# Kernel tuning notes

Measured on AMD Instinct MI355X. Metric: run time of the kernel, lower is better.

## Reference

```python
import jax, jax.numpy as jnp
import numpy as np

B, T, F_DIM, HID, CH = 16, 4096, 47, 64, 256  # batch, frames, feature_dim, hidden_feature_dim, num_channels


def setup_inputs() -> dict:
    key = jax.random.key(0)
    ks = jax.random.split(key, 8)
    s = 0.08  # weight scale
    return {
        "features": jax.random.normal(ks[0], (B, T, F_DIM), jnp.float32),
        # conv1: Conv1d(47, 64, k=1) -> pointwise linear, torch weight (out,in,1) squeezed
        "W1": jax.random.normal(ks[1], (HID, F_DIM), jnp.float32) * s,
        "b1": jnp.zeros((HID,), jnp.float32),
        # conv2: Conv1d(256, 256, k=2), torch weight (out, in, k)
        "W2": jax.random.normal(ks[2], (CH, 4 * HID, 2), jnp.float32) * s,
        "b2": jnp.zeros((CH,), jnp.float32),
        # tconv: ConvTranspose1d(256, 256, k=4, stride=4), torch weight (in, out, k)
        "Wt": jax.random.normal(ks[3], (CH, CH, 4), jnp.float32) * s,
        "bt": jnp.zeros((CH,), jnp.float32),
        # GRU(256, 256), torch layout: (3*H, in) with gate order [r, z, n]
        "W_ih": jax.random.normal(ks[4], (3 * CH, CH), jnp.float32) * s,
        "W_hh": jax.random.normal(ks[5], (3 * CH, CH), jnp.float32) * s,
        "b_ih": jnp.zeros((3 * CH,), jnp.float32),
        "b_hh": jnp.zeros((3 * CH,), jnp.float32),
    }


def reference(features, W1, b1, W2, b2, Wt, bt, W_ih, W_hh, b_ih, b_hh):
    b, t = features.shape[0], features.shape[1]
    ch = Wt.shape[1]
    # conv1 (k=1) == pointwise linear + tanh: (B,T,47) -> (B,T,64)
    c = jnp.tanh(jnp.einsum('btf,hf->bth', features, W1) + b1)
    # group 4 frames: (B, T/4, 256)
    c = c.reshape(b, t // 4, -1)
    # conv2 k=2 with left pad 1 (causal): y[t] = W2[..0] x[t-1] + W2[..1] x[t]
    cp = jnp.pad(c, ((0, 0), (1, 0), (0, 0)))
    c = jnp.tanh(jnp.einsum('bti,oi->bto', cp[:, :-1], W2[:, :, 0])
                 + jnp.einsum('bti,oi->bto', cp[:, 1:], W2[:, :, 1]) + b2)
    # tconv: stride-4 transpose conv, k=4 -> each frame emits 4 steps
    c = jnp.tanh(jnp.einsum('bti,iok->btko', c, Wt) + bt)  # (B, T/4, 4, CH)
    c = c.reshape(b, t, ch)
    # GRU (torch semantics, gate order r,z,n); precompute input projections
    gates_x = jnp.einsum('btc,gc->btg', c, W_ih) + b_ih  # (B,T,3CH)

    def step(h, gx):
        gh = h @ W_hh.T + b_hh
        xr, xz, xn = jnp.split(gx, 3, axis=-1)
        hr, hz, hn = jnp.split(gh, 3, axis=-1)
        r = jax.nn.sigmoid(xr + hr)
        z = jax.nn.sigmoid(xz + hz)
        n = jnp.tanh(xn + r * hn)
        h = (1 - z) * n + z * h
        return h, h

    h0 = jnp.zeros((b, ch), features.dtype)
    _, hs = jax.lax.scan(step, h0, jnp.swapaxes(gates_x, 0, 1))  # (T,B,CH)
    return jnp.swapaxes(hs, 0, 1)  # (B,T,CH)
```

## Files before the change

### kernel.cpp

```cpp
#include <hip/hip_runtime.h>
#include <hip/hip_bf16.h>
#include <stdint.h>

#define B_   16
#define T_   4096
#define F_   47
#define HID_ 64
#define CH_  256
#define TG_  1024
#define G3_  768

using bf16x8 = __attribute__((ext_vector_type(8))) short;
using f32x4  = __attribute__((ext_vector_type(4))) float;

__device__ __forceinline__ short f2bf(float f) {
    union { float f; uint32_t u; } v; v.f = f;
    uint32_t u = v.u;
    uint32_t r = (u + 0x7fffu + ((u >> 16) & 1u)) >> 16;
    return (short)r;
}
__device__ __forceinline__ float bf2f(short s) {
    union { uint32_t u; float f; } v; v.u = ((uint32_t)(uint16_t)s) << 16;
    return v.f;
}
__device__ __forceinline__ float fast_tanh(float x) {
    float e = __expf(2.f * x);
    return 1.f - 2.f / (e + 1.f);
}
__device__ __forceinline__ float fast_sigmoid(float x) {
    return 1.f / (1.f + __expf(-x));
}

__global__ __launch_bounds__(256) void k1_conv1(const float* __restrict__ feat,
        const float* __restrict__ W1, const float* __restrict__ b1,
        short* __restrict__ c1) {
    __shared__ float sW[47 * 64];
    __shared__ float sF[4 * 47];
    int tid = threadIdx.x;
    int b = blockIdx.x >> 10, t0 = (blockIdx.x & 1023) * 4;
    if (tid < 188) sF[tid] = feat[((size_t)b * T_ + t0) * 47 + tid];
    for (int i = tid; i < 47 * 64; i += 256) {
        int f = i >> 6, h = i & 63;
        sW[i] = W1[h * 47 + f];
    }
    __syncthreads();
    int fr = tid >> 6, h = tid & 63;
    float acc = b1[h];
    #pragma unroll
    for (int f = 0; f < 47; ++f)
        acc += sF[fr * 47 + f] * sW[f * 64 + h];
    c1[((size_t)b * T_ + t0 + fr) * 64 + h] = f2bf(fast_tanh(acc));
}

__global__ __launch_bounds__(256) void k_prep(const float* __restrict__ W2,
        const float* __restrict__ Wt, const float* __restrict__ Wih_f,
        short* __restrict__ W2t, short* __restrict__ Wtt, short* __restrict__ Wih) {
    int idx = blockIdx.x * 256 + threadIdx.x;
    if (idx < 256 * 512) {
        int o = idx >> 9, i = idx & 511, d = i >> 8, j = i & 255;
        W2t[idx] = f2bf(W2[(size_t)o * 512 + j * 2 + d]);
    }
    {
        int n = idx >> 8, ic = idx & 255, o = n & 255, kp = n >> 8;
        Wtt[idx] = f2bf(Wt[(size_t)ic * 1024 + o * 4 + kp]);
    }
    if (idx < G3_ * CH_)
        Wih[idx] = f2bf(Wih_f[idx]);
}

__global__ __launch_bounds__(256) void k2_conv2(const short* __restrict__ c1,
        const short* __restrict__ W2t, const float* __restrict__ b2,
        short* __restrict__ y2) {
    int tid = threadIdx.x, w = tid >> 6, l = tid & 63;
    int lane16 = l & 15, quad = l >> 4;
    int mt = blockIdx.x * 4 + w;
    int row = mt * 16 + lane16;
    int tg = row & 1023;
    const short* Arow = c1 + (size_t)row * 256 - 256;
    bf16x8 zero8 = {0,0,0,0,0,0,0,0};
    bf16x8 af[16];
    #pragma unroll
    for (int kt = 0; kt < 16; ++kt) {
        int i0 = kt * 32 + quad * 8;
        bool masked = (tg == 0) && (kt < 8);
        const short* p = masked ? c1 : (Arow + i0);
        bf16x8 v = *(const bf16x8*)p;
        af[kt] = masked ? zero8 : v;
    }
    #pragma unroll
    for (int nt = 0; nt < 16; ++nt) {
        int n = nt * 16 + lane16;
        f32x4 acc = {0.f, 0.f, 0.f, 0.f};
        const short* Brow = W2t + (size_t)n * 512 + quad * 8;
        #pragma unroll
        for (int kt = 0; kt < 16; ++kt) {
            bf16x8 bf = *(const bf16x8*)(Brow + kt * 32);
            acc = __builtin_amdgcn_mfma_f32_16x16x32_bf16(af[kt], bf, acc, 0, 0, 0);
        }
        float bias = b2[n];
        #pragma unroll
        for (int r = 0; r < 4; ++r) {
            int mrow = mt * 16 + quad * 4 + r;
            y2[(size_t)mrow * 256 + n] = f2bf(fast_tanh(acc[r] + bias));
        }
    }
}

__global__ __launch_bounds__(256) void k3a_tconv(const short* __restrict__ y2,
        const short* __restrict__ Wtt, const float* __restrict__ bt,
        short* __restrict__ c3) {
    int tid = threadIdx.x, w = tid >> 6, l = tid & 63;
    int lane16 = l & 15, quad = l >> 4;
    int mt = blockIdx.x;
    int row = mt * 16 + lane16;
    const short* Arow = y2 + (size_t)row * 256 + quad * 8;
    bf16x8 af[8];
    #pragma unroll
    for (int kt = 0; kt < 8; ++kt) af[kt] = *(const bf16x8*)(Arow + kt * 32);
    #pragma unroll
    for (int nt2 = 0; nt2 < 16; ++nt2) {
        int n = (w * 16 + nt2) * 16 + lane16;
        f32x4 acc = {0.f, 0.f, 0.f, 0.f};
        const short* Brow = Wtt + (size_t)n * 256 + quad * 8;
        #pragma unroll
        for (int kt = 0; kt < 8; ++kt) {
            bf16x8 bf = *(const bf16x8*)(Brow + kt * 32);
            acc = __builtin_amdgcn_mfma_f32_16x16x32_bf16(af[kt], bf, acc, 0, 0, 0);
        }
        int kp = n >> 8, o = n & 255;
        float bias = bt[o];
        #pragma unroll
        for (int r = 0; r < 4; ++r) {
            int mrow = mt * 16 + quad * 4 + r;
            int bb = mrow >> 10, tgg = mrow & 1023;
            c3[(((size_t)bb * TG_ + tgg) * 4 + kp) * 256 + o] =
                f2bf(fast_tanh(acc[r] + bias));
        }
    }
}

__global__ __launch_bounds__(256) void k3b_xproj(const short* __restrict__ c3,
        const short* __restrict__ Wih, const float* __restrict__ b_ih,
        short* __restrict__ gates) {
    int tid = threadIdx.x, w = tid >> 6, l = tid & 63;
    int lane16 = l & 15, quad = l >> 4;
    int mt = blockIdx.x;
    int row = mt * 16 + lane16;
    const short* Arow = c3 + (size_t)row * 256 + quad * 8;
    bf16x8 af[8];
    #pragma unroll
    for (int kt = 0; kt < 8; ++kt) af[kt] = *(const bf16x8*)(Arow + kt * 32);
    #pragma unroll
    for (int nt2 = 0; nt2 < 12; ++nt2) {
        int n = (w * 12 + nt2) * 16 + lane16;
        f32x4 acc = {0.f, 0.f, 0.f, 0.f};
        const short* Brow = Wih + (size_t)n * 256 + quad * 8;
        #pragma unroll
        for (int kt = 0; kt < 8; ++kt) {
            bf16x8 bf = *(const bf16x8*)(Brow + kt * 32);
            acc = __builtin_amdgcn_mfma_f32_16x16x32_bf16(af[kt], bf, acc, 0, 0, 0);
        }
        float bias = b_ih[n];
        #pragma unroll
        for (int r = 0; r < 4; ++r) {
            int mrow = mt * 16 + quad * 4 + r;
            gates[(size_t)mrow * G3_ + n] = f2bf(acc[r] + bias);
        }
    }
}

__global__ __launch_bounds__(512, 2) void k4_gru(const float* __restrict__ W_hh,
        const float* __restrict__ b_hh, const short* __restrict__ gates,
        float* __restrict__ out) {
    __shared__ __align__(16) short h_bf[256];
    __shared__ float gh[G3_];
    __shared__ __align__(16) short gxb[2][8][G3_];
    __shared__ __align__(16) float ob[8][256];
    int tid = threadIdx.x, l = tid & 63;
    int w = tid >> 6;
    int lane16 = l & 15, quad = l >> 4;
    int b = blockIdx.x;

    bf16x8 Bfr[6][8];
    #pragma unroll
    for (int t = 0; t < 6; ++t) {
        int n = (w * 6 + t) * 16 + lane16;
        const float* p = W_hh + (size_t)n * 256 + quad * 8;
        #pragma unroll
        for (int kt = 0; kt < 8; ++kt) {
            const f32x4* q = (const f32x4*)(p + kt * 32);
            f32x4 u0 = q[0], u1 = q[1];
            bf16x8 v;
            v[0] = f2bf(u0[0]); v[1] = f2bf(u0[1]); v[2] = f2bf(u0[2]); v[3] = f2bf(u0[3]);
            v[4] = f2bf(u1[0]); v[5] = f2bf(u1[1]); v[6] = f2bf(u1[2]); v[7] = f2bf(u1[3]);
            Bfr[t][kt] = v;
        }
    }

    float h_reg = 0.f, bhr = 0.f, bhz = 0.f, bhn = 0.f;
    if (tid < 256) {
        h_bf[tid] = 0;
        bhr = b_hh[tid]; bhz = b_hh[256 + tid]; bhn = b_hh[512 + tid];
    }
    const uint32_t* gxg = (const uint32_t*)(gates + (size_t)b * T_ * G3_);
    if (tid < 384) {
        #pragma unroll
        for (int j = 0; j < 8; ++j)
            ((uint32_t*)&gxb[0][j][0])[tid] = gxg[(size_t)j * 384 + tid];
    }
    __syncthreads();

    float* outb = out + (size_t)b * T_ * CH_;
    uint32_t r[8];
    for (int s = 0; s < T_; ++s) {
        bool ldq = ((s & 7) == 0) && (s + 8 < T_) && (tid < 384);
        if (ldq) {
            #pragma unroll
            for (int j = 0; j < 8; ++j)
                r[j] = gxg[(size_t)(s + 8 + j) * 384 + tid];
        }

        f32x4 acc[6];
        #pragma unroll
        for (int t = 0; t < 6; ++t) acc[t] = (f32x4){0.f, 0.f, 0.f, 0.f};
        bf16x8 af[4];
        #pragma unroll
        for (int p = 0; p < 4; ++p)
            af[p] = *(const bf16x8*)&h_bf[p * 32 + quad * 8];
        #pragma unroll
        for (int kt = 0; kt < 8; ++kt) {
            bf16x8 a = af[kt & 3];
            if (kt + 4 < 8)
                af[kt & 3] = *(const bf16x8*)&h_bf[(kt + 4) * 32 + quad * 8];
            #pragma unroll
            for (int t = 0; t < 6; ++t)
                acc[t] = __builtin_amdgcn_mfma_f32_16x16x32_bf16(a, Bfr[t][kt], acc[t], 0, 0, 0);
        }
        if (l < 16) {
            #pragma unroll
            for (int t = 0; t < 6; ++t) gh[(w * 6 + t) * 16 + l] = acc[t][0];
        }
        __syncthreads();

        if (ldq) {
            int half = ((s >> 3) + 1) & 1;
            #pragma unroll
            for (int j = 0; j < 8; ++j)
                ((uint32_t*)&gxb[half][j][0])[tid] = r[j];
        }

        if (tid < 256) {
            const short* gx = &gxb[(s >> 3) & 1][s & 7][0];
            float hr = gh[tid] + bhr;
            float hz = gh[256 + tid] + bhz;
            float hn = gh[512 + tid] + bhn;
            float xr = bf2f(gx[tid]), xz = bf2f(gx[256 + tid]), xn = bf2f(gx[512 + tid]);
            float rg = fast_sigmoid(xr + hr);
            float z = fast_sigmoid(xz + hz);
            float nn = fast_tanh(xn + rg * hn);
            h_reg = (1.f - z) * nn + z * h_reg;
            h_bf[tid] = f2bf(h_reg);
            ob[s & 7][tid] = h_reg;
        }
        __syncthreads();

        if ((s & 7) == 7) {
            f32x4 v = *(const f32x4*)&ob[0][tid * 4];
            *(f32x4*)&outb[(size_t)(s - 7) * 256 + tid * 4] = v;
        }
    }
}

extern "C" void kernel_launch(void* const* d_in, const int* in_sizes, int n_in,
                              void* d_out, int out_size, void* d_ws, size_t ws_size,
                              hipStream_t stream) {
    const float* feat  = (const float*)d_in[0];
    const float* W1    = (const float*)d_in[1];
    const float* b1    = (const float*)d_in[2];
    const float* W2    = (const float*)d_in[3];
    const float* b2    = (const float*)d_in[4];
    const float* Wt    = (const float*)d_in[5];
    const float* bt    = (const float*)d_in[6];
    const float* Wih_f = (const float*)d_in[7];
    const float* Whh   = (const float*)d_in[8];
    const float* bhh   = (const float*)d_in[10];
    const float* bih   = (const float*)d_in[9];
    float* out = (float*)d_out;

    char* ws = (char*)d_ws;
    short* c3    = (short*)(ws);
    short* c1    = (short*)(ws);
    short* gates = (short*)(ws + 33554432);
    short* y2    = (short*)(ws + 33554432);
    short* W2t   = (short*)(ws + 134217728);
    short* Wtt   = (short*)(ws + 134217728 + 262144);
    short* Wih   = (short*)(ws + 134217728 + 262144 + 524288);

    k1_conv1 <<<16384, 256, 0, stream>>>(feat, W1, b1, c1);
    k_prep   <<<1024, 256, 0, stream>>>(W2, Wt, Wih_f, W2t, Wtt, Wih);
    k2_conv2 <<<256,  256, 0, stream>>>(c1, W2t, b2, y2);
    k3a_tconv<<<1024, 256, 0, stream>>>(y2, Wtt, bt, c3);
    k3b_xproj<<<4096, 256, 0, stream>>>(c3, Wih, bih, gates);
    k4_gru   <<<16,   512, 0, stream>>>(Whh, bhh, gates, out);
}
```

Baseline: 5.678 ms.

## Replace MFMA GRU recurrence with fp16 dot2 per-thread matvec and LDS-direct prefetch

```diff
diff --git a/kernel.cpp b/kernel.cpp
--- a/kernel.cpp
+++ b/kernel.cpp
@@ -12,6 +12,8 @@
 
 using bf16x8 = __attribute__((ext_vector_type(8))) short;
 using f32x4  = __attribute__((ext_vector_type(4))) float;
+using f16x8  = __attribute__((ext_vector_type(8))) _Float16;
+using h2     = __attribute__((ext_vector_type(2))) _Float16;
 
 __device__ __forceinline__ short f2bf(float f) {
     union { float f; uint32_t u; } v; v.f = f;
@@ -30,6 +32,26 @@
 __device__ __forceinline__ float fast_sigmoid(float x) {
     return 1.f / (1.f + __expf(-x));
 }
+
+#if __has_builtin(__builtin_amdgcn_fdot2)
+#define FDOT2(a, b, c) __builtin_amdgcn_fdot2((a), (b), (c), false)
+#else
+__device__ __forceinline__ float fdot2_emul(h2 a, h2 b, float c) {
+    return c + (float)a[0] * (float)b[0] + (float)a[1] * (float)b[1];
+}
+#define FDOT2(a, b, c) fdot2_emul((a), (b), (c))
+#endif
+
+#if __has_builtin(__builtin_amdgcn_global_load_lds)
+#define HAS_GLL 1
+__device__ __forceinline__ void gl_lds16(const void* g, void* l) {
+    __builtin_amdgcn_global_load_lds(
+        (const __attribute__((address_space(1))) uint32_t*)g,
+        (__attribute__((address_space(3))) uint32_t*)l, 16, 0, 0);
+}
+#else
+#define HAS_GLL 0
+#endif
 
 __global__ __launch_bounds__(256) void k1_conv1(const float* __restrict__ feat,
         const float* __restrict__ W1, const float* __restrict__ b1,
@@ -57,8 +79,8 @@
         short* __restrict__ W2t, short* __restrict__ Wtt, short* __restrict__ Wih) {
     int idx = blockIdx.x * 256 + threadIdx.x;
     if (idx < 256 * 512) {
-        int o = idx >> 9, i = idx & 511, d = i >> 8, j = i & 255;
-        W2t[idx] = f2bf(W2[(size_t)o * 512 + j * 2 + d]);
+        int o = idx >> 9, i = idx & 511, d = i >> 8, jj = i & 255;
+        W2t[idx] = f2bf(W2[(size_t)o * 512 + jj * 2 + d]);
     }
     {
         int n = idx >> 8, ic = idx & 255, o = n & 255, kp = n >> 8;
@@ -169,104 +191,125 @@
     }
 }
 
-__global__ __launch_bounds__(512, 2) void k4_gru(const float* __restrict__ W_hh,
+__global__ __launch_bounds__(512) void k4_gru_dot2(const float* __restrict__ W_hh,
         const float* __restrict__ b_hh, const short* __restrict__ gates,
         float* __restrict__ out) {
-    __shared__ __align__(16) short h_bf[256];
-    __shared__ float gh[G3_];
     __shared__ __align__(16) short gxb[2][8][G3_];
-    __shared__ __align__(16) float ob[8][256];
-    int tid = threadIdx.x, l = tid & 63;
-    int w = tid >> 6;
-    int lane16 = l & 15, quad = l >> 4;
+    __shared__ __align__(16) float part[G3_ * 4];
+    __shared__ __align__(16) float ob[8 * 256];
+    __shared__ __align__(16) short hq_s[4 * 72];
+
+    int tid = threadIdx.x, l = tid & 63, w = tid >> 6;
+    int q = tid & 3, n0 = tid >> 2;
     int b = blockIdx.x;
 
-    bf16x8 Bfr[6][8];
-    #pragma unroll
-    for (int t = 0; t < 6; ++t) {
-        int n = (w * 6 + t) * 16 + lane16;
-        const float* p = W_hh + (size_t)n * 256 + quad * 8;
-        #pragma unroll
-        for (int kt = 0; kt < 8; ++kt) {
-            const f32x4* q = (const f32x4*)(p + kt * 32);
-            f32x4 u0 = q[0], u1 = q[1];
-            bf16x8 v;
-            v[0] = f2bf(u0[0]); v[1] = f2bf(u0[1]); v[2] = f2bf(u0[2]); v[3] = f2bf(u0[3]);
-            v[4] = f2bf(u1[0]); v[5] = f2bf(u1[1]); v[6] = f2bf(u1[2]); v[7] = f2bf(u1[3]);
-            Bfr[t][kt] = v;
+    h2 wreg[6][32];
+    #pragma unroll
+    for (int k = 0; k < 6; ++k) {
+        const float2* row = (const float2*)(W_hh + ((size_t)(n0 + k * 128)) * 256 + q * 64);
+        #pragma unroll
+        for (int j = 0; j < 32; ++j) {
+            float2 v = row[j];
+            h2 p; p[0] = (_Float16)v.x; p[1] = (_Float16)v.y;
+            wreg[k][j] = p;
         }
     }
 
     float h_reg = 0.f, bhr = 0.f, bhz = 0.f, bhn = 0.f;
     if (tid < 256) {
-        h_bf[tid] = 0;
         bhr = b_hh[tid]; bhz = b_hh[256 + tid]; bhn = b_hh[512 + tid];
     }
-    const uint32_t* gxg = (const uint32_t*)(gates + (size_t)b * T_ * G3_);
-    if (tid < 384) {
-        #pragma unroll
-        for (int j = 0; j < 8; ++j)
-            ((uint32_t*)&gxb[0][j][0])[tid] = gxg[(size_t)j * 384 + tid];
-    }
+    if (tid < 288) hq_s[tid] = 0;
+
+    const short* gbase = gates + (size_t)b * T_ * G3_;
+    const char* gbytes = (const char*)gbase;
+
+#if HAS_GLL
+    {
+        char* dst = (char*)&gxb[0][0][0];
+        gl_lds16(gbytes + w * 1024 + l * 16, dst + w * 1024);
+        if (w < 4) gl_lds16(gbytes + (8 + w) * 1024 + l * 16, dst + (8 + w) * 1024);
+    }
+#else
+    {
+        const uint32_t* g32 = (const uint32_t*)gbytes;
+        uint32_t* d = (uint32_t*)&gxb[0][0][0];
+        #pragma unroll
+        for (int i = 0; i < 6; ++i) d[tid + i * 512] = g32[tid + i * 512];
+    }
+#endif
     __syncthreads();
 
     float* outb = out + (size_t)b * T_ * CH_;
-    uint32_t r[8];
     for (int s = 0; s < T_; ++s) {
-        bool ldq = ((s & 7) == 0) && (s + 8 < T_) && (tid < 384);
-        if (ldq) {
+        bool grp0 = ((s & 7) == 0) && (s + 8 < T_);
+#if HAS_GLL
+        if (grp0) {
+            const char* src = gbytes + (size_t)(s + 8) * 1536;
+            char* dst = (char*)&gxb[((s >> 3) + 1) & 1][0][0];
+            gl_lds16(src + w * 1024 + l * 16, dst + w * 1024);
+            if (w < 4) gl_lds16(src + (8 + w) * 1024 + l * 16, dst + (8 + w) * 1024);
+        }
+#else
+        uint32_t pf[6];
+        if (grp0) {
+            const uint32_t* src = (const uint32_t*)(gbytes + (size_t)(s + 8) * 1536);
             #pragma unroll
-            for (int j = 0; j < 8; ++j)
-                r[j] = gxg[(size_t)(s + 8 + j) * 384 + tid];
-        }
-
-        f32x4 acc[6];
-        #pragma unroll
-        for (int t = 0; t < 6; ++t) acc[t] = (f32x4){0.f, 0.f, 0.f, 0.f};
-        bf16x8 af[4];
-        #pragma unroll
-        for (int p = 0; p < 4; ++p)
-            af[p] = *(const bf16x8*)&h_bf[p * 32 + quad * 8];
-        #pragma unroll
-        for (int kt = 0; kt < 8; ++kt) {
-            bf16x8 a = af[kt & 3];
-            if (kt + 4 < 8)
-                af[kt & 3] = *(const bf16x8*)&h_bf[(kt + 4) * 32 + quad * 8];
+            for (int i = 0; i < 6; ++i) pf[i] = src[tid + i * 512];
+        }
+#endif
+
+        h2 hq[32];
+        #pragma unroll
+        for (int g2 = 0; g2 < 8; ++g2) {
+            f16x8 v = *(const f16x8*)&hq_s[q * 72 + g2 * 8];
             #pragma unroll
-            for (int t = 0; t < 6; ++t)
-                acc[t] = __builtin_amdgcn_mfma_f32_16x16x32_bf16(a, Bfr[t][kt], acc[t], 0, 0, 0);
-        }
-        if (l < 16) {
+            for (int p2 = 0; p2 < 4; ++p2) {
+                h2 p; p[0] = v[p2 * 2]; p[1] = v[p2 * 2 + 1];
+                hq[g2 * 4 + p2] = p;
+            }
+        }
+        float acc[6] = {0.f, 0.f, 0.f, 0.f, 0.f, 0.f};
+        #pragma unroll
+        for (int j = 0; j < 32; ++j) {
             #pragma unroll
-            for (int t = 0; t < 6; ++t) gh[(w * 6 + t) * 16 + l] = acc[t][0];
-        }
+            for (int k = 0; k < 6; ++k)
+                acc[k] = FDOT2(wreg[k][j], hq[j], acc[k]);
+        }
+        #pragma unroll
+        for (int k = 0; k < 6; ++k)
+            part[(n0 + k * 128) * 4 + q] = acc[k];
         __syncthreads();
 
-        if (ldq) {
-            int half = ((s >> 3) + 1) & 1;
+#if !HAS_GLL
+        if (grp0) {
+            uint32_t* d = (uint32_t*)&gxb[((s >> 3) + 1) & 1][0][0];
             #pragma unroll
-            for (int j = 0; j < 8; ++j)
-                ((uint32_t*)&gxb[half][j][0])[tid] = r[j];
-        }
-
+            for (int i = 0; i < 6; ++i) d[tid + i * 512] = pf[i];
+        }
+#endif
         if (tid < 256) {
             const short* gx = &gxb[(s >> 3) & 1][s & 7][0];
-            float hr = gh[tid] + bhr;
-            float hz = gh[256 + tid] + bhz;
-            float hn = gh[512 + tid] + bhn;
+            f32x4 pr = *(const f32x4*)&part[tid * 4];
+            f32x4 pz = *(const f32x4*)&part[(256 + tid) * 4];
+            f32x4 pn = *(const f32x4*)&part[(512 + tid) * 4];
+            float gr = (pr[0] + pr[1]) + (pr[2] + pr[3]);
+            float gz = (pz[0] + pz[1]) + (pz[2] + pz[3]);
+            float gn = (pn[0] + pn[1]) + (pn[2] + pn[3]);
             float xr = bf2f(gx[tid]), xz = bf2f(gx[256 + tid]), xn = bf2f(gx[512 + tid]);
-            float rg = fast_sigmoid(xr + hr);
-            float z = fast_sigmoid(xz + hz);
-            float nn = fast_tanh(xn + rg * hn);
+            float r = fast_sigmoid(xr + gr + bhr);
+            float z = fast_sigmoid(xz + gz + bhz);
+            float nn = fast_tanh(xn + r * (gn + bhn));
             h_reg = (1.f - z) * nn + z * h_reg;
-            h_bf[tid] = f2bf(h_reg);
-            ob[s & 7][tid] = h_reg;
+            union { _Float16 f; short u; } cv; cv.f = (_Float16)h_reg;
+            hq_s[(tid >> 6) * 72 + (tid & 63)] = cv.u;
+            ob[(s & 7) * 256 + tid] = h_reg;
         }
         __syncthreads();
 
         if ((s & 7) == 7) {
-            f32x4 v = *(const f32x4*)&ob[0][tid * 4];
-            *(f32x4*)&outb[(size_t)(s - 7) * 256 + tid * 4] = v;
+            f32x4 v = *(const f32x4*)&ob[tid * 4];
+            *(f32x4*)&outb[(size_t)(s - 7 + (tid >> 6)) * 256 + (tid & 63) * 4] = v;
         }
     }
 }
@@ -283,8 +326,8 @@
     const float* bt    = (const float*)d_in[6];
     const float* Wih_f = (const float*)d_in[7];
     const float* Whh   = (const float*)d_in[8];
+    const float* bih   = (const float*)d_in[9];
     const float* bhh   = (const float*)d_in[10];
-    const float* bih   = (const float*)d_in[9];
     float* out = (float*)d_out;
 
     char* ws = (char*)d_ws;
@@ -296,10 +339,10 @@
     short* Wtt   = (short*)(ws + 134217728 + 262144);
     short* Wih   = (short*)(ws + 134217728 + 262144 + 524288);
 
-    k1_conv1 <<<16384, 256, 0, stream>>>(feat, W1, b1, c1);
-    k_prep   <<<1024, 256, 0, stream>>>(W2, Wt, Wih_f, W2t, Wtt, Wih);
-    k2_conv2 <<<256,  256, 0, stream>>>(c1, W2t, b2, y2);
-    k3a_tconv<<<1024, 256, 0, stream>>>(y2, Wtt, bt, c3);
-    k3b_xproj<<<4096, 256, 0, stream>>>(c3, Wih, bih, gates);
-    k4_gru   <<<16,   512, 0, stream>>>(Whh, bhh, gates, out);
-}
+    k1_conv1   <<<16384, 256, 0, stream>>>(feat, W1, b1, c1);
+    k_prep     <<<1024, 256, 0, stream>>>(W2, Wt, Wih_f, W2t, Wtt, Wih);
+    k2_conv2   <<<256,  256, 0, stream>>>(c1, W2t, b2, y2);
+    k3a_tconv  <<<1024, 256, 0, stream>>>(y2, Wtt, bt, c3);
+    k3b_xproj  <<<4096, 256, 0, stream>>>(c3, Wih, bih, gates);
+    k4_gru_dot2<<<16,   512, 0, stream>>>(Whh, bhh, gates, out);
+}
```

New measurement: 5.223 ms. -8.0%, faster.
